# Performance work log

Measured on AMD Instinct MI355X. Metric: run time of the kernel, lower is better.

Reference implementation:

```python
import jax, jax.numpy as jnp
import numpy as np

B, L, V, D, H = 4096, 32, 50000, 300, 6
HD = D // H  # 50


def setup_inputs() -> dict:
    key = jax.random.key(0)
    ks = jax.random.split(key, 9)
    s = 0.02
    return {
        "title": jax.random.randint(ks[0], (B, L), 0, V),
        "emb": jax.random.normal(ks[1], (V, D), dtype=jnp.float32) * s,
        "pos_emb": jax.random.normal(ks[2], (512, D), dtype=jnp.float32) * s,
        "Wq": jax.random.normal(ks[3], (D, D), dtype=jnp.float32) * s,
        "bq": jnp.zeros((D,), jnp.float32),
        "Wk": jax.random.normal(ks[4], (D, D), dtype=jnp.float32) * s,
        "bk": jnp.zeros((D,), jnp.float32),
        "Wv": jax.random.normal(ks[5], (D, D), dtype=jnp.float32) * s,
        "bv": jnp.zeros((D,), jnp.float32),
        "Wo": jax.random.normal(ks[6], (D, D), dtype=jnp.float32) * s,
        "bo": jnp.zeros((D,), jnp.float32),
        "Va": jax.random.normal(ks[7], (D, D), dtype=jnp.float32) * s,
        "ba": jnp.zeros((D,), jnp.float32),
        "qw": jax.random.normal(ks[8], (D, 1), dtype=jnp.float32) * s,
    }


def reference(title, emb, pos_emb, Wq, bq, Wk, bk, Wv, bv, Wo, bo, Va, ba, qw):
    b, l = title.shape
    # word embedding + positional embedding
    x = emb[title] + pos_emb[:l][None, :, :]  # [B, L, D]

    def heads(y):  # [B, L, D] -> [B, H, L, HD]
        return y.reshape(b, l, H, HD).transpose(0, 2, 1, 3)

    # manual multi-head self-attention (mask is all-ones -> no masking effect)
    q = heads(x @ Wq.T + bq) / jnp.sqrt(jnp.float32(HD))
    k = heads(x @ Wk.T + bk)
    v = heads(x @ Wv.T + bv)
    scores = jnp.einsum("bhqd,bhkd->bhqk", q, k)  # [B, H, L, L]
    w = jax.nn.softmax(scores, axis=-1)  # dropout is identity in eval
    ctx = jnp.einsum("bhqk,bhkd->bhqd", w, v)
    ctx = ctx.transpose(0, 2, 1, 3).reshape(b, l, D)
    ctx = ctx @ Wo.T + bo  # [B, L, D]

    # additive attention pooling
    t = jnp.tanh(ctx @ Va.T + ba)          # [B, L, D]
    a = (t @ qw)[..., 0]                    # [B, L]
    alpha = jax.nn.softmax(a, axis=1)       # [B, L]
    out = jnp.einsum("bs,bsd->bd", alpha, ctx)  # [B, D]
    return out
```

## Files before the change

kernel.cpp:

```cpp
#include <hip/hip_runtime.h>
#include <math.h>

typedef _Float16 f16;
typedef _Float16 half8 __attribute__((ext_vector_type(8)));
typedef _Float16 half4 __attribute__((ext_vector_type(4)));
typedef float float4v __attribute__((ext_vector_type(4)));
typedef int int4v __attribute__((ext_vector_type(4)));

#define MFMA16(a, b, c) __builtin_amdgcn_mfma_f32_16x16x32_f16((a), (b), (c), 0, 0, 0)


#define WQKV_OFF 0u
#define BQKV_OFF 655360u
#define WO_OFF   659456u
#define WVA_OFF  864256u
#define BVA_OFF  1069056u

__device__ __forceinline__ float fast_tanh(float x) {
    float e = __expf(2.f * x);
    return 1.f - 2.f / (e + 1.f);
}

__global__ __launch_bounds__(256) void repack_all(
    const float* __restrict__ Wq, const float* __restrict__ Wk,
    const float* __restrict__ Wv, const float* __restrict__ Wo,
    const float* __restrict__ bq, const float* __restrict__ bk,
    const float* __restrict__ bv, const float* __restrict__ Va,
    const float* __restrict__ bo, const float* __restrict__ ba,
    f16* __restrict__ wqkvF, f16* __restrict__ wo16F, float* __restrict__ bqkv,
    f16* __restrict__ wvaF, float* __restrict__ bva) {
    const int bid = blockIdx.x, tid = threadIdx.x;
    const float rs = 0.14142135623730951f;
    if (bid < 1684) {
        int idx = bid * 256 + tid;
        if (idx < 327680) {
            int ntile = idx / 5120, rem = idx - ntile * 5120;
            int ks = rem / 512, r2 = rem - ks * 512;
            int lane = r2 >> 3, j = r2 & 7;
            int n = ntile * 16 + (lane & 15);
            int k = ks * 32 + (lane >> 4) * 8 + j;
            int g = n / 320, r = n - g * 320;
            float v = 0.f;
            if (r < 300 && k < 300) {
                if (g == 0) v = Wq[r * 300 + k] * rs;
                else if (g == 1) v = Wk[r * 300 + k];
                else if (g == 2) v = Wv[r * 300 + k];
            }
            wqkvF[idx] = (f16)v;
        } else if (idx < 430080) {
            int t = idx - 327680;
            int ntile = t / 5120, rem = t - ntile * 5120;
            int ks = rem / 512, r2 = rem - ks * 512;
            int lane = r2 >> 3, j = r2 & 7;
            int n = ntile * 16 + (lane & 15);
            int k = ks * 32 + (lane >> 4) * 8 + j;
            wo16F[t] = (f16)((n < 300 && k < 300) ? Wo[n * 300 + k] : 0.f);
        } else if (idx < 431104) {
            int n = idx - 430080;
            int g = n / 320, r = n - g * 320;
            float v = 0.f;
            if (r < 300) {
                if (g == 0) v = bq[r] * rs;
                else if (g == 1) v = bk[r];
                else if (g == 2) v = bv[r];
            }
            bqkv[n] = v;
        }
    } else if (bid < 1784) {
        int bt = (bid - 1684) * 4 + (tid >> 6);
        int mt = bt / 20, nt = bt % 20;
        int lane = tid & 63;
        int lr = lane & 15, quad = lane >> 4;
        float4v acc = {0.f, 0.f, 0.f, 0.f};
        int m = mt * 16 + lr;
        int nn = nt * 16 + lr;
        for (int ks = 0; ks < 10; ++ks) {
            int c = ks * 32 + quad * 8;
            half8 af, bf;
#pragma unroll
            for (int j = 0; j < 8; ++j) {
                int cc = c + j;
                af[j] = (f16)((m < 300 && cc < 300) ? Va[m * 300 + cc] : 0.f);
                bf[j] = (f16)((nn < 300 && cc < 300) ? Wo[cc * 300 + nn] : 0.f);
            }
            acc = MFMA16(af, bf, acc);
        }
#pragma unroll
        for (int r = 0; r < 4; ++r) {
            int row = mt * 16 + quad * 4 + r;
            int col = nt * 16 + lr;
            int addr = ((row >> 4) * 10 + (col >> 5)) * 512 +
                       (((col >> 3) & 3) * 16 + (row & 15)) * 8 + (col & 7);
            wvaF[addr] = (f16)acc[r];
        }
    } else {
        int j = (bid - 1784) * 4 + (tid >> 6);
        int lane = tid & 63;
        float s = 0.f;
        if (j < 300) {
            for (int k = lane; k < 300; k += 64) s += Va[j * 300 + k] * bo[k];
        }
#pragma unroll
        for (int off = 1; off < 64; off <<= 1) s += __shfl_xor(s, off, 64);
        if (lane == 0) bva[j] = (j < 300) ? s + ba[j] : 0.f;
    }
}

__global__ __launch_bounds__(512, 4) void qkvattn_kernel(
    const int* __restrict__ title, const float* __restrict__ emb,
    const float* __restrict__ pos,
    const f16* __restrict__ wqkvF, const float* __restrict__ bqkv,
    const f16* __restrict__ wvaF, const float* __restrict__ bva,
    const float* __restrict__ qw, const f16* __restrict__ wo16F,
    const float* __restrict__ bo, float* __restrict__ out) {
    __shared__ __align__(16) f16 qL[6 * 32 * 72];
    __shared__ __align__(16) f16 kL[6 * 32 * 72];
    __shared__ __align__(16) f16 vT[6 * 64 * 32];
    __shared__ __align__(16) f16 cbarL[320];
    __shared__ float aL[32];
    const int ib = blockIdx.x, tid = threadIdx.x;
    const int w = tid >> 6, lane = tid & 63, lr = lane & 15, quad = lane >> 4;
    const float4v vz = {0.f, 0.f, 0.f, 0.f};
    const int4v z4 = {0, 0, 0, 0};
    f16* xA = vT;

    int tt[3];
#pragma unroll
    for (int ii = 0; ii < 3; ++ii) {
        int u = tid + ii * 512;
        if (u < 1280) {
            int lu = u & 63;
            int row = ((u >> 6) / 10) * 16 + (lu & 15);
            tt[ii] = title[ib * 32 + row];
        }
    }
#pragma unroll
    for (int ii = 0; ii < 3; ++ii) {
        int u = tid + ii * 512;
        if (u < 1280) {
            int fragblk = u >> 6, lu = u & 63;
            int mt = fragblk / 10, ks = fragblk - mt * 10;
            int row = mt * 16 + (lu & 15);
            int col = ks * 32 + (lu >> 4) * 8;
            int t = tt[ii];
            half8 h;
            if (col + 8 <= 300) {
                float4v e0 = *(const float4v*)&emb[t * 300 + col];
                float4v e1 = *(const float4v*)&emb[t * 300 + col + 4];
                float4v p0 = *(const float4v*)&pos[row * 300 + col];
                float4v p1 = *(const float4v*)&pos[row * 300 + col + 4];
#pragma unroll
                for (int j = 0; j < 4; ++j) {
                    h[j] = (f16)(e0[j] + p0[j]);
                    h[4 + j] = (f16)(e1[j] + p1[j]);
                }
            } else {
#pragma unroll
                for (int j = 0; j < 8; ++j) {
                    int cc = col + j;
                    h[j] = (f16)((cc < 300) ? emb[t * 300 + cc] + pos[row * 300 + cc] : 0.f);
                }
            }
            *(half8*)&xA[u * 8] = h;
        }
    }
    for (int i = tid; i < 1344; i += 512) {
        int hrow = i / 7, c = i - hrow * 7;
        ((int*)&qL[hrow * 72 + 50])[c] = 0;
        ((int*)&kL[hrow * 72 + 50])[c] = 0;
    }
    if (tid < 32) aL[tid] = 0.f;
    float bb[8];
#pragma unroll
    for (int j = 0; j < 8; ++j) bb[j] = bqkv[(w * 8 + j) * 16 + lr];
    __syncthreads();

    float4v acc[2][8];
#pragma unroll
    for (int mt = 0; mt < 2; ++mt)
#pragma unroll
        for (int j = 0; j < 8; ++j) acc[mt][j] = vz;
#pragma unroll
    for (int ks = 0; ks < 10; ++ks) {
        half8 a0 = *(const half8*)&xA[(ks * 64 + lane) * 8];
        half8 a1 = *(const half8*)&xA[((10 + ks) * 64 + lane) * 8];
#pragma unroll
        for (int j = 0; j < 8; ++j) {
            int tile = w * 8 + j;
            if (tile < 60) {
                half8 bf = *(const half8*)&wqkvF[((tile * 10 + ks) * 64 + lane) * 8];
                acc[0][j] = MFMA16(a0, bf, acc[0][j]);
                acc[1][j] = MFMA16(a1, bf, acc[1][j]);
            }
        }
    }
    __syncthreads();

    for (int i = tid; i < 336; i += 512) {
        int t = i >> 2, c4 = i & 3;
        int h = t / 14, d = 50 + (t - (t / 14) * 14);
        ((int4v*)&vT[(h * 64 + d) * 32])[c4] = z4;
    }
#pragma unroll
    for (int j = 0; j < 8; ++j) {
        int tile = w * 8 + j;
        int wi = tile / 20;
        int n = tile * 16 + lr;
        int cc = n - wi * 320;
        if (wi < 3 && cc < 300) {
            int h = cc / 50, d = cc - h * 50;
            if (wi == 2) {
#pragma unroll
                for (int mt = 0; mt < 2; ++mt) {
                    int row0 = mt * 16 + quad * 4;
                    half4 pk;
#pragma unroll
                    for (int r = 0; r < 4; ++r) pk[r] = (f16)(acc[mt][j][r] + bb[j]);
                    int idx = (h * 64 + d) * 32 + row0;
                    int byt = (idx * 2) ^ (((d >> 2) & 3) << 4);
                    *(half4*)((char*)vT + byt) = pk;
                }
            } else {
                f16* dst = (wi == 0) ? qL : kL;
#pragma unroll
                for (int mt = 0; mt < 2; ++mt)
#pragma unroll
                    for (int r = 0; r < 4; ++r) {
                        int row = mt * 16 + quad * 4 + r;
                        dst[(h * 32 + row) * 72 + d] = (f16)(acc[mt][j][r] + bb[j]);
                    }
            }
        }
    }
    __syncthreads();

    const int hh = w;
    if (w < 6) {
        float4v s00 = vz, s01 = vz, s10 = vz, s11 = vz;
#pragma unroll
        for (int ks = 0; ks < 2; ++ks) {
            int c = ks * 32 + quad * 8;
            half8 aq0 = *(const half8*)&qL[(hh * 32 + lr) * 72 + c];
            half8 aq1 = *(const half8*)&qL[(hh * 32 + 16 + lr) * 72 + c];
            half8 bk0 = *(const half8*)&kL[(hh * 32 + lr) * 72 + c];
            half8 bk1 = *(const half8*)&kL[(hh * 32 + 16 + lr) * 72 + c];
            s00 = MFMA16(aq0, bk0, s00);
            s01 = MFMA16(aq0, bk1, s01);
            s10 = MFMA16(aq1, bk0, s10);
            s11 = MFMA16(aq1, bk1, s11);
        }
        f16* ph = qL + hh * 32 * 72;
#pragma unroll
        for (int mt = 0; mt < 2; ++mt) {
            float4v sv0 = mt ? s10 : s00;
            float4v sv1 = mt ? s11 : s01;
#pragma unroll
            for (int r = 0; r < 4; ++r) {
                float v0 = sv0[r], v1 = sv1[r];
                float m = fmaxf(v0, v1);
#pragma unroll
                for (int off = 1; off < 16; off <<= 1) m = fmaxf(m, __shfl_xor(m, off, 64));
                float e0 = __expf(v0 - m), e1 = __expf(v1 - m);
                float ss = e0 + e1;
#pragma unroll
                for (int off = 1; off < 16; off <<= 1) ss += __shfl_xor(ss, off, 64);
                float inv = 1.0f / ss;
                int row = mt * 16 + quad * 4 + r;
                ph[row * 40 + lr] = (f16)(e0 * inv);
                ph[row * 40 + 16 + lr] = (f16)(e1 * inv);
            }
        }
    }
    __syncthreads();

    f16* scratch = kL;
    for (int i = tid; i < 32 * 28; i += 512) {
        int row = i / 28, cc = 300 + (i - row * 28);
        scratch[row * 328 + cc] = (f16)0.f;
    }
    if (w < 6) {
        int h = hh;
        f16* ph = qL + hh * 32 * 72;
        half8 aw0 = *(const half8*)&ph[lr * 40 + quad * 8];
        half8 aw1 = *(const half8*)&ph[(16 + lr) * 40 + quad * 8];
        float4v c0[4], c1[4];
#pragma unroll
        for (int nt = 0; nt < 4; ++nt) { c0[nt] = vz; c1[nt] = vz; }
#pragma unroll
        for (int nt = 0; nt < 4; ++nt) {
            int rIdx = nt * 16 + lr;
            int idx = (hh * 64 + rIdx) * 32 + quad * 8;
            int byt = (idx * 2) ^ (((rIdx >> 2) & 3) << 4);
            half8 bvf = *(const half8*)((const char*)vT + byt);
            c0[nt] = MFMA16(aw0, bvf, c0[nt]);
            c1[nt] = MFMA16(aw1, bvf, c1[nt]);
        }
#pragma unroll
        for (int mt = 0; mt < 2; ++mt)
#pragma unroll
            for (int nt = 0; nt < 4; ++nt)
#pragma unroll
                for (int r = 0; r < 4; ++r) {
                    int d = nt * 16 + lr;
                    if (d < 50) {
                        int row = mt * 16 + quad * 4 + r;
                        float4v cv = mt ? c1[nt] : c0[nt];
                        scratch[row * 328 + h * 50 + d] = (f16)cv[r];
                    }
                }
    }

    const int mtile = w >> 2, nsub = w & 3;
    half8 pbf[5];
    float pbva[5], pqw[5];
#pragma unroll
    for (int i = 0; i < 5; ++i) {
        int n = (nsub * 5 + i) * 16 + lr;
        pbf[i] = *(const half8*)&wvaF[(((nsub * 5 + i) * 10) * 64 + lane) * 8];
        pbva[i] = bva[n];
        pqw[i] = (n < 300) ? qw[n] : 0.f;
    }
    __syncthreads();

    {
        float4v vacc[5];
#pragma unroll
        for (int i = 0; i < 5; ++i) vacc[i] = vz;
        const int arow = (mtile * 16 + lr) * 328;
        {
            half8 a = *(const half8*)&scratch[arow + quad * 8];
#pragma unroll
            for (int i = 0; i < 5; ++i) vacc[i] = MFMA16(a, pbf[i], vacc[i]);
        }
#pragma unroll
        for (int ks = 1; ks < 10; ++ks) {
            half8 a = *(const half8*)&scratch[arow + ks * 32 + quad * 8];
#pragma unroll
            for (int i = 0; i < 5; ++i) {
                half8 bf = *(const half8*)&wvaF[((((nsub * 5 + i) * 10) + ks) * 64 + lane) * 8];
                vacc[i] = MFMA16(a, bf, vacc[i]);
            }
        }
        float ps[4] = {0.f, 0.f, 0.f, 0.f};
#pragma unroll
        for (int i = 0; i < 5; ++i) {
#pragma unroll
            for (int r = 0; r < 4; ++r) ps[r] += fast_tanh(vacc[i][r] + pbva[i]) * pqw[i];
        }
#pragma unroll
        for (int r = 0; r < 4; ++r)
#pragma unroll
            for (int off = 1; off < 16; off <<= 1) ps[r] += __shfl_xor(ps[r], off, 64);
        if (lr == 0) {
#pragma unroll
            for (int r = 0; r < 4; ++r) atomicAdd(&aL[mtile * 16 + quad * 4 + r], ps[r]);
        }
    }
    __syncthreads();

    {
        float av = aL[lane & 31];
        float m5 = av;
#pragma unroll
        for (int off = 1; off < 32; off <<= 1) m5 = fmaxf(m5, __shfl_xor(m5, off, 32));
        float e5 = __expf(av - m5);
        float ss5 = e5;
#pragma unroll
        for (int off = 1; off < 32; off <<= 1) ss5 += __shfl_xor(ss5, off, 32);
        float al = e5 / ss5;
        if (tid < 320) {
            int d = tid;
            float acc6 = 0.f;
#pragma unroll
            for (int l = 0; l < 32; ++l)
                acc6 += __shfl(al, l, 32) * (float)scratch[l * 328 + d];
            cbarL[d] = (f16)acc6;
        }
    }
    __syncthreads();

    {
        half8 af[10];
#pragma unroll
        for (int ks = 0; ks < 10; ++ks)
            af[ks] = *(const half8*)&cbarL[ks * 32 + quad * 8];
        for (int t = w; t < 19; t += 8) {
            float4v oacc = vz;
#pragma unroll
            for (int ks = 0; ks < 10; ++ks) {
                half8 bf = *(const half8*)&wo16F[((t * 10 + ks) * 64 + lane) * 8];
                oacc = MFMA16(af[ks], bf, oacc);
            }
            int n = t * 16 + lr;
            if (quad == 0 && n < 300) out[ib * 300 + n] = oacc[0] + bo[n];
        }
    }
}

extern "C" void kernel_launch(void* const* d_in, const int* in_sizes, int n_in,
                              void* d_out, int out_size, void* d_ws, size_t ws_size,
                              hipStream_t stream) {
    const int* title = (const int*)d_in[0];
    const float* emb = (const float*)d_in[1];
    const float* pos = (const float*)d_in[2];
    const float* Wq = (const float*)d_in[3];
    const float* bq = (const float*)d_in[4];
    const float* Wk = (const float*)d_in[5];
    const float* bk = (const float*)d_in[6];
    const float* Wv = (const float*)d_in[7];
    const float* bv = (const float*)d_in[8];
    const float* Wo = (const float*)d_in[9];
    const float* bo = (const float*)d_in[10];
    const float* Va = (const float*)d_in[11];
    const float* ba = (const float*)d_in[12];
    const float* qw = (const float*)d_in[13];
    char* ws = (char*)d_ws;
    float* out = (float*)d_out;

    f16* wqkvF = (f16*)(ws + WQKV_OFF);
    float* bqkv = (float*)(ws + BQKV_OFF);
    f16* wo16F = (f16*)(ws + WO_OFF);
    f16* wvaF = (f16*)(ws + WVA_OFF);
    float* bva = (float*)(ws + BVA_OFF);

    repack_all<<<1864, 256, 0, stream>>>(Wq, Wk, Wv, Wo, bq, bk, bv, Va, bo, ba,
                                         wqkvF, wo16F, bqkv, wvaF, bva);
    qkvattn_kernel<<<4096, 512, 0, stream>>>(title, emb, pos, wqkvF, bqkv, wvaF, bva,
                                             qw, wo16F, bo, out);
}
```

Baseline: 449.6 us.

## Split output projection into batched kernel, double-buffer weight loads, skip padding tiles

The final Wo projection moves out of the per-sample kernel into a separate out_kernel that processes 16 pooled vectors per block, so the MFMA M-dimension is used fully instead of one row of 16. The QKV and Va GEMM loops now double-buffer B-fragment loads from global memory (even/odd k-steps) and skip the all-padding column tiles 19/39/59. The Va stage is re-split so each wave covers both 16-row tiles with 2-3 column tiles, which reuses each weight fragment across two MFMAs. This adds a workspace round trip for the pooled vectors in fp16 and one extra kernel launch.

```diff
diff --git a/kernel.cpp b/kernel.cpp
--- a/kernel.cpp
+++ b/kernel.cpp
@@ -15,6 +15,7 @@
 #define WO_OFF   659456u
 #define WVA_OFF  864256u
 #define BVA_OFF  1069056u
+#define CBAR_OFF 1070336u
 
 __device__ __forceinline__ float fast_tanh(float x) {
     float e = __expf(2.f * x);
@@ -111,12 +112,10 @@
     const float* __restrict__ pos,
     const f16* __restrict__ wqkvF, const float* __restrict__ bqkv,
     const f16* __restrict__ wvaF, const float* __restrict__ bva,
-    const float* __restrict__ qw, const f16* __restrict__ wo16F,
-    const float* __restrict__ bo, float* __restrict__ out) {
+    const float* __restrict__ qw, f16* __restrict__ cbar) {
     __shared__ __align__(16) f16 qL[6 * 32 * 72];
     __shared__ __align__(16) f16 kL[6 * 32 * 72];
     __shared__ __align__(16) f16 vT[6 * 64 * 32];
-    __shared__ __align__(16) f16 cbarL[320];
     __shared__ float aL[32];
     const int ib = blockIdx.x, tid = threadIdx.x;
     const int w = tid >> 6, lane = tid & 63, lr = lane & 15, quad = lane >> 4;
@@ -181,17 +180,45 @@
 #pragma unroll
         for (int j = 0; j < 8; ++j) acc[mt][j] = vz;
 #pragma unroll
-    for (int ks = 0; ks < 10; ++ks) {
-        half8 a0 = *(const half8*)&xA[(ks * 64 + lane) * 8];
-        half8 a1 = *(const half8*)&xA[((10 + ks) * 64 + lane) * 8];
-#pragma unroll
-        for (int j = 0; j < 8; ++j) {
-            int tile = w * 8 + j;
-            if (tile < 60) {
-                half8 bf = *(const half8*)&wqkvF[((tile * 10 + ks) * 64 + lane) * 8];
-                acc[0][j] = MFMA16(a0, bf, acc[0][j]);
-                acc[1][j] = MFMA16(a1, bf, acc[1][j]);
-            }
+    for (int g = 0; g < 2; ++g) {
+        const int tb = w * 8 + g * 4;
+        bool vld[4];
+#pragma unroll
+        for (int i = 0; i < 4; ++i) {
+            int t = tb + i;
+            vld[i] = (t < 60) && (t != 19) && (t != 39) && (t != 59);
+        }
+        const f16* bp = wqkvF + tb * 5120 + lane * 8;
+        half8 e[4], o[4];
+#pragma unroll
+        for (int i = 0; i < 4; ++i)
+            if (vld[i]) e[i] = *(const half8*)(bp + i * 5120);
+#pragma unroll
+        for (int ks = 0; ks < 10; ks += 2) {
+#pragma unroll
+            for (int i = 0; i < 4; ++i)
+                if (vld[i]) o[i] = *(const half8*)(bp + i * 5120 + (ks + 1) * 512);
+            half8 a0 = *(const half8*)&xA[(ks * 64 + lane) * 8];
+            half8 a1 = *(const half8*)&xA[((10 + ks) * 64 + lane) * 8];
+#pragma unroll
+            for (int i = 0; i < 4; ++i)
+                if (vld[i]) {
+                    acc[0][g * 4 + i] = MFMA16(a0, e[i], acc[0][g * 4 + i]);
+                    acc[1][g * 4 + i] = MFMA16(a1, e[i], acc[1][g * 4 + i]);
+                }
+            if (ks + 2 < 10) {
+#pragma unroll
+                for (int i = 0; i < 4; ++i)
+                    if (vld[i]) e[i] = *(const half8*)(bp + i * 5120 + (ks + 2) * 512);
+            }
+            half8 a2 = *(const half8*)&xA[((ks + 1) * 64 + lane) * 8];
+            half8 a3 = *(const half8*)&xA[((11 + ks) * 64 + lane) * 8];
+#pragma unroll
+            for (int i = 0; i < 4; ++i)
+                if (vld[i]) {
+                    acc[0][g * 4 + i] = MFMA16(a2, o[i], acc[0][g * 4 + i]);
+                    acc[1][g * 4 + i] = MFMA16(a3, o[i], acc[1][g * 4 + i]);
+                }
         }
     }
     __syncthreads();
@@ -310,50 +337,77 @@
                 }
     }
 
-    const int mtile = w >> 2, nsub = w & 3;
-    half8 pbf[5];
-    float pbva[5], pqw[5];
-#pragma unroll
-    for (int i = 0; i < 5; ++i) {
-        int n = (nsub * 5 + i) * 16 + lr;
-        pbf[i] = *(const half8*)&wvaF[(((nsub * 5 + i) * 10) * 64 + lane) * 8];
-        pbva[i] = bva[n];
-        pqw[i] = (n < 300) ? qw[n] : 0.f;
-    }
+    const int NT = (w < 4) ? 3 : 2;
+    const int tb4 = (w < 4) ? w * 3 : 12 + (w - 4) * 2;
+    const f16* vp = wvaF + tb4 * 5120 + lane * 8;
+    half8 e4[3], o4[3];
+    float pbva[3], pqw[3];
+#pragma unroll
+    for (int i = 0; i < 3; ++i)
+        if (i < NT) {
+            int n = (tb4 + i) * 16 + lr;
+            e4[i] = *(const half8*)(vp + i * 5120);
+            pbva[i] = bva[n];
+            pqw[i] = (n < 300) ? qw[n] : 0.f;
+        }
     __syncthreads();
 
     {
-        float4v vacc[5];
-#pragma unroll
-        for (int i = 0; i < 5; ++i) vacc[i] = vz;
-        const int arow = (mtile * 16 + lr) * 328;
-        {
-            half8 a = *(const half8*)&scratch[arow + quad * 8];
-#pragma unroll
-            for (int i = 0; i < 5; ++i) vacc[i] = MFMA16(a, pbf[i], vacc[i]);
-        }
-#pragma unroll
-        for (int ks = 1; ks < 10; ++ks) {
-            half8 a = *(const half8*)&scratch[arow + ks * 32 + quad * 8];
-#pragma unroll
-            for (int i = 0; i < 5; ++i) {
-                half8 bf = *(const half8*)&wvaF[((((nsub * 5 + i) * 10) + ks) * 64 + lane) * 8];
-                vacc[i] = MFMA16(a, bf, vacc[i]);
-            }
-        }
-        float ps[4] = {0.f, 0.f, 0.f, 0.f};
-#pragma unroll
-        for (int i = 0; i < 5; ++i) {
-#pragma unroll
-            for (int r = 0; r < 4; ++r) ps[r] += fast_tanh(vacc[i][r] + pbva[i]) * pqw[i];
-        }
-#pragma unroll
-        for (int r = 0; r < 4; ++r)
-#pragma unroll
-            for (int off = 1; off < 16; off <<= 1) ps[r] += __shfl_xor(ps[r], off, 64);
+        float4v vacc[2][3];
+#pragma unroll
+        for (int mt = 0; mt < 2; ++mt)
+#pragma unroll
+            for (int i = 0; i < 3; ++i) vacc[mt][i] = vz;
+#pragma unroll
+        for (int ks = 0; ks < 10; ks += 2) {
+#pragma unroll
+            for (int i = 0; i < 3; ++i)
+                if (i < NT) o4[i] = *(const half8*)(vp + i * 5120 + (ks + 1) * 512);
+            half8 a0 = *(const half8*)&scratch[lr * 328 + ks * 32 + quad * 8];
+            half8 a1 = *(const half8*)&scratch[(16 + lr) * 328 + ks * 32 + quad * 8];
+#pragma unroll
+            for (int i = 0; i < 3; ++i)
+                if (i < NT) {
+                    vacc[0][i] = MFMA16(a0, e4[i], vacc[0][i]);
+                    vacc[1][i] = MFMA16(a1, e4[i], vacc[1][i]);
+                }
+            if (ks + 2 < 10) {
+#pragma unroll
+                for (int i = 0; i < 3; ++i)
+                    if (i < NT) e4[i] = *(const half8*)(vp + i * 5120 + (ks + 2) * 512);
+            }
+            half8 a2 = *(const half8*)&scratch[lr * 328 + (ks + 1) * 32 + quad * 8];
+            half8 a3 = *(const half8*)&scratch[(16 + lr) * 328 + (ks + 1) * 32 + quad * 8];
+#pragma unroll
+            for (int i = 0; i < 3; ++i)
+                if (i < NT) {
+                    vacc[0][i] = MFMA16(a2, o4[i], vacc[0][i]);
+                    vacc[1][i] = MFMA16(a3, o4[i], vacc[1][i]);
+                }
+        }
+        float ps[2][4] = {{0.f, 0.f, 0.f, 0.f}, {0.f, 0.f, 0.f, 0.f}};
+#pragma unroll
+        for (int i = 0; i < 3; ++i)
+            if (i < NT) {
+#pragma unroll
+                for (int mt = 0; mt < 2; ++mt)
+#pragma unroll
+                    for (int r = 0; r < 4; ++r)
+                        ps[mt][r] += fast_tanh(vacc[mt][i][r] + pbva[i]) * pqw[i];
+            }
+#pragma unroll
+        for (int mt = 0; mt < 2; ++mt)
+#pragma unroll
+            for (int r = 0; r < 4; ++r)
+#pragma unroll
+                for (int off = 1; off < 16; off <<= 1)
+                    ps[mt][r] += __shfl_xor(ps[mt][r], off, 64);
         if (lr == 0) {
 #pragma unroll
-            for (int r = 0; r < 4; ++r) atomicAdd(&aL[mtile * 16 + quad * 4 + r], ps[r]);
+            for (int mt = 0; mt < 2; ++mt)
+#pragma unroll
+                for (int r = 0; r < 4; ++r)
+                    atomicAdd(&aL[mt * 16 + quad * 4 + r], ps[mt][r]);
         }
     }
     __syncthreads();
@@ -374,25 +428,37 @@
 #pragma unroll
             for (int l = 0; l < 32; ++l)
                 acc6 += __shfl(al, l, 32) * (float)scratch[l * 328 + d];
-            cbarL[d] = (f16)acc6;
-        }
-    }
-    __syncthreads();
-
-    {
-        half8 af[10];
-#pragma unroll
-        for (int ks = 0; ks < 10; ++ks)
-            af[ks] = *(const half8*)&cbarL[ks * 32 + quad * 8];
-        for (int t = w; t < 19; t += 8) {
-            float4v oacc = vz;
-#pragma unroll
-            for (int ks = 0; ks < 10; ++ks) {
-                half8 bf = *(const half8*)&wo16F[((t * 10 + ks) * 64 + lane) * 8];
-                oacc = MFMA16(af[ks], bf, oacc);
-            }
-            int n = t * 16 + lr;
-            if (quad == 0 && n < 300) out[ib * 300 + n] = oacc[0] + bo[n];
+            cbar[ib * 320 + d] = (f16)acc6;
+        }
+    }
+}
+
+__global__ __launch_bounds__(512) void out_kernel(
+    const f16* __restrict__ cbar, const f16* __restrict__ wo16F,
+    const float* __restrict__ bo, float* __restrict__ out) {
+    __shared__ __align__(16) f16 cA[16 * 328];
+    const int mb = blockIdx.x, tid = threadIdx.x;
+    const int w = tid >> 6, lane = tid & 63, lr = lane & 15, quad = lane >> 4;
+    for (int i = tid; i < 640; i += 512) {
+        int row = i / 40, g = i - row * 40;
+        *(half8*)&cA[row * 328 + g * 8] = *(const half8*)&cbar[(mb * 16 + row) * 320 + g * 8];
+    }
+    __syncthreads();
+    const float4v vz = {0.f, 0.f, 0.f, 0.f};
+    for (int t = w; t < 19; t += 8) {
+        float4v acc = vz;
+#pragma unroll
+        for (int ks = 0; ks < 10; ++ks) {
+            half8 a = *(const half8*)&cA[lr * 328 + ks * 32 + quad * 8];
+            half8 bf = *(const half8*)&wo16F[((t * 10 + ks) * 64 + lane) * 8];
+            acc = MFMA16(a, bf, acc);
+        }
+        int n = t * 16 + lr;
+        if (n < 300) {
+            float bb = bo[n];
+#pragma unroll
+            for (int r = 0; r < 4; ++r)
+                out[(mb * 16 + quad * 4 + r) * 300 + n] = acc[r] + bb;
         }
     }
 }
@@ -422,9 +488,11 @@
     f16* wo16F = (f16*)(ws + WO_OFF);
     f16* wvaF = (f16*)(ws + WVA_OFF);
     float* bva = (float*)(ws + BVA_OFF);
+    f16* cbar = (f16*)(ws + CBAR_OFF);
 
     repack_all<<<1864, 256, 0, stream>>>(Wq, Wk, Wv, Wo, bq, bk, bv, Va, bo, ba,
                                          wqkvF, wo16F, bqkv, wvaF, bva);
     qkvattn_kernel<<<4096, 512, 0, stream>>>(title, emb, pos, wqkvF, bqkv, wvaF, bva,
-                                             qw, wo16F, bo, out);
+                                             qw, cbar);
+    out_kernel<<<256, 512, 0, stream>>>(cbar, wo16F, bo, out);
 }
```

New measurement: 849.7 us. +89.0%, slower.

## Split final Wo projection into a separate batched MFMA kernel

Applied to the files above, without the earlier changes.

The per-sample output projection (pooled context times Wo) is moved out of the fused attention kernel. The attention kernel now writes the pooled f16 context to workspace, and a new kernel multiplies 16 samples at a time so all MFMA rows are used instead of one. The embedding-gather prologue is also simplified from a two-phase token prefetch into a single loop. The cost is an extra kernel launch and a global round trip for the pooled vectors.

```diff
diff --git a/kernel.cpp b/kernel.cpp
--- a/kernel.cpp
+++ b/kernel.cpp
@@ -15,6 +15,7 @@
 #define WO_OFF   659456u
 #define WVA_OFF  864256u
 #define BVA_OFF  1069056u
+#define CBAR_OFF 1070336u
 
 __device__ __forceinline__ float fast_tanh(float x) {
     float e = __expf(2.f * x);
@@ -111,12 +112,10 @@
     const float* __restrict__ pos,
     const f16* __restrict__ wqkvF, const float* __restrict__ bqkv,
     const f16* __restrict__ wvaF, const float* __restrict__ bva,
-    const float* __restrict__ qw, const f16* __restrict__ wo16F,
-    const float* __restrict__ bo, float* __restrict__ out) {
+    const float* __restrict__ qw, f16* __restrict__ cbar) {
     __shared__ __align__(16) f16 qL[6 * 32 * 72];
     __shared__ __align__(16) f16 kL[6 * 32 * 72];
     __shared__ __align__(16) f16 vT[6 * 64 * 32];
-    __shared__ __align__(16) f16 cbarL[320];
     __shared__ float aL[32];
     const int ib = blockIdx.x, tid = threadIdx.x;
     const int w = tid >> 6, lane = tid & 63, lr = lane & 15, quad = lane >> 4;
@@ -124,45 +123,31 @@
     const int4v z4 = {0, 0, 0, 0};
     f16* xA = vT;
 
-    int tt[3];
-#pragma unroll
-    for (int ii = 0; ii < 3; ++ii) {
-        int u = tid + ii * 512;
-        if (u < 1280) {
-            int lu = u & 63;
-            int row = ((u >> 6) / 10) * 16 + (lu & 15);
-            tt[ii] = title[ib * 32 + row];
-        }
-    }
-#pragma unroll
-    for (int ii = 0; ii < 3; ++ii) {
-        int u = tid + ii * 512;
-        if (u < 1280) {
-            int fragblk = u >> 6, lu = u & 63;
-            int mt = fragblk / 10, ks = fragblk - mt * 10;
-            int row = mt * 16 + (lu & 15);
-            int col = ks * 32 + (lu >> 4) * 8;
-            int t = tt[ii];
-            half8 h;
-            if (col + 8 <= 300) {
-                float4v e0 = *(const float4v*)&emb[t * 300 + col];
-                float4v e1 = *(const float4v*)&emb[t * 300 + col + 4];
-                float4v p0 = *(const float4v*)&pos[row * 300 + col];
-                float4v p1 = *(const float4v*)&pos[row * 300 + col + 4];
-#pragma unroll
-                for (int j = 0; j < 4; ++j) {
-                    h[j] = (f16)(e0[j] + p0[j]);
-                    h[4 + j] = (f16)(e1[j] + p1[j]);
-                }
-            } else {
-#pragma unroll
-                for (int j = 0; j < 8; ++j) {
-                    int cc = col + j;
-                    h[j] = (f16)((cc < 300) ? emb[t * 300 + cc] + pos[row * 300 + cc] : 0.f);
-                }
-            }
-            *(half8*)&xA[u * 8] = h;
-        }
+    for (int u = tid; u < 1280; u += 512) {
+        int fragblk = u >> 6, lu = u & 63;
+        int mt = fragblk / 10, ks = fragblk - mt * 10;
+        int row = mt * 16 + (lu & 15);
+        int col = ks * 32 + (lu >> 4) * 8;
+        int t = title[ib * 32 + row];
+        half8 h;
+        if (col + 8 <= 300) {
+            float4v e0 = *(const float4v*)&emb[t * 300 + col];
+            float4v e1 = *(const float4v*)&emb[t * 300 + col + 4];
+            float4v p0 = *(const float4v*)&pos[row * 300 + col];
+            float4v p1 = *(const float4v*)&pos[row * 300 + col + 4];
+#pragma unroll
+            for (int j = 0; j < 4; ++j) {
+                h[j] = (f16)(e0[j] + p0[j]);
+                h[4 + j] = (f16)(e1[j] + p1[j]);
+            }
+        } else {
+#pragma unroll
+            for (int j = 0; j < 8; ++j) {
+                int cc = col + j;
+                h[j] = (f16)((cc < 300) ? emb[t * 300 + cc] + pos[row * 300 + cc] : 0.f);
+            }
+        }
+        *(half8*)&xA[u * 8] = h;
     }
     for (int i = tid; i < 1344; i += 512) {
         int hrow = i / 7, c = i - hrow * 7;
@@ -374,25 +359,37 @@
 #pragma unroll
             for (int l = 0; l < 32; ++l)
                 acc6 += __shfl(al, l, 32) * (float)scratch[l * 328 + d];
-            cbarL[d] = (f16)acc6;
-        }
-    }
-    __syncthreads();
-
-    {
-        half8 af[10];
-#pragma unroll
-        for (int ks = 0; ks < 10; ++ks)
-            af[ks] = *(const half8*)&cbarL[ks * 32 + quad * 8];
-        for (int t = w; t < 19; t += 8) {
-            float4v oacc = vz;
-#pragma unroll
-            for (int ks = 0; ks < 10; ++ks) {
-                half8 bf = *(const half8*)&wo16F[((t * 10 + ks) * 64 + lane) * 8];
-                oacc = MFMA16(af[ks], bf, oacc);
-            }
-            int n = t * 16 + lr;
-            if (quad == 0 && n < 300) out[ib * 300 + n] = oacc[0] + bo[n];
+            cbar[ib * 320 + d] = (f16)acc6;
+        }
+    }
+}
+
+__global__ __launch_bounds__(512) void out_kernel(
+    const f16* __restrict__ cbar, const f16* __restrict__ wo16F,
+    const float* __restrict__ bo, float* __restrict__ out) {
+    __shared__ __align__(16) f16 cA[16 * 328];
+    const int mb = blockIdx.x, tid = threadIdx.x;
+    const int w = tid >> 6, lane = tid & 63, lr = lane & 15, quad = lane >> 4;
+    for (int i = tid; i < 640; i += 512) {
+        int row = i / 40, g = i - row * 40;
+        *(half8*)&cA[row * 328 + g * 8] = *(const half8*)&cbar[(mb * 16 + row) * 320 + g * 8];
+    }
+    __syncthreads();
+    const float4v vz = {0.f, 0.f, 0.f, 0.f};
+    for (int t = w; t < 19; t += 8) {
+        float4v acc = vz;
+#pragma unroll
+        for (int ks = 0; ks < 10; ++ks) {
+            half8 a = *(const half8*)&cA[lr * 328 + ks * 32 + quad * 8];
+            half8 bf = *(const half8*)&wo16F[((t * 10 + ks) * 64 + lane) * 8];
+            acc = MFMA16(a, bf, acc);
+        }
+        int n = t * 16 + lr;
+        if (n < 300) {
+            float bb = bo[n];
+#pragma unroll
+            for (int r = 0; r < 4; ++r)
+                out[(mb * 16 + quad * 4 + r) * 300 + n] = acc[r] + bb;
         }
     }
 }
@@ -422,9 +419,11 @@
     f16* wo16F = (f16*)(ws + WO_OFF);
     f16* wvaF = (f16*)(ws + WVA_OFF);
     float* bva = (float*)(ws + BVA_OFF);
+    f16* cbar = (f16*)(ws + CBAR_OFF);
 
     repack_all<<<1864, 256, 0, stream>>>(Wq, Wk, Wv, Wo, bq, bk, bv, Va, bo, ba,
                                          wqkvF, wo16F, bqkv, wvaF, bva);
     qkvattn_kernel<<<4096, 512, 0, stream>>>(title, emb, pos, wqkvF, bqkv, wvaF, bva,
-                                             qw, wo16F, bo, out);
+                                             qw, cbar);
+    out_kernel<<<256, 512, 0, stream>>>(cbar, wo16F, bo, out);
 }
```

Measured after the change: 425.1 us. 1.06x faster.
